# Kernel tuning notes

Measured on AMD Instinct MI355X. Metric: run time of the kernel, lower is better.

The kernel has to match this reference:

```python
import jax, jax.numpy as jnp
import numpy as np

H, N_EMB, D_EMB, D_UP = 1024, 8192, 512, 2048
B, T, BB, M, K_LABELS = 4, 4096, 512, 4096, 64


def _rms(x, w, eps=1e-6):
    xf = x.astype(jnp.float32)
    var = jnp.mean(xf * xf, axis=-1, keepdims=True)
    return (w * (xf * jax.lax.rsqrt(var + eps))).astype(x.dtype)


def setup_inputs() -> dict:
    key = jax.random.key(0)
    ks = jax.random.split(key, 8)
    bt = B * T
    inp = jax.random.normal(ks[0], (B, T, H), jnp.float32)
    w_k = jax.random.normal(ks[1], (N_EMB, H), jnp.float32) * 0.02
    w_v = jax.random.normal(ks[2], (N_EMB, D_EMB), jnp.float32) * 0.02
    w_up = jax.random.normal(ks[3], (D_UP, D_EMB), jnp.float32) * 0.02
    w_mix = jax.random.normal(ks[4], (H, D_UP + H), jnp.float32) * 0.02
    fw = jax.random.permutation(ks[5], bt)
    bw = jnp.argsort(fw)  # inverse permutation
    seq_sort = jax.random.randint(ks[6], (bt,), 0, K_LABELS)
    keep_cols = jnp.arange(M)  # keep first M of N_EMB rows
    emb_alloc = jnp.arange(N_EMB) % K_LABELS  # every label present among kept rows
    starts = jnp.zeros((bt,), jnp.int32)
    ends = jnp.full((bt,), M, jnp.int32)
    return {
        'input': inp, 'fw': fw, 'bw': bw, 'seq_sort': seq_sort,
        'keep_cols': keep_cols, 'emb_alloc': emb_alloc,
        'starts': starts, 'ends': ends, 'bb': BB,
        'w_k_weight': w_k, 'w_v_weight': w_v, 'w_up_weight': w_up,
        'w_mix_weight': w_mix,
        'norm_in_weight': jnp.ones((H,), jnp.float32),
        'norm_out_weight': jnp.ones((D_UP,), jnp.float32),
    }


def reference(input, fw, bw, seq_sort, keep_cols, emb_alloc, starts, ends, bb,
              w_k_weight, w_v_weight, w_up_weight, w_mix_weight,
              norm_in_weight, norm_out_weight):
    b, t, h = input.shape
    A = _rms(input, norm_in_weight)                      # [b,t,h]
    Bm = w_k_weight[keep_cols]                           # [m,h]
    Cm = w_v_weight[keep_cols]                           # [m,d_emb]
    la = emb_alloc[keep_cols]                            # [m]
    A = A.reshape(-1, h)[fw].reshape(-1, bb, h)          # [nb,bb,h]
    ss = seq_sort.reshape(-1, bb)                        # [nb,bb]
    st = starts.reshape(-1, bb).min(axis=-1)             # [nb]
    en = ends.reshape(-1, bb).max(axis=-1)               # [nb]
    # ragged per-block slice B[start:end] expressed as a kv range mask,
    # combined with the equality mask seq_sort[q] == emb_alloc[kv]
    scores = jnp.einsum('nqh,kh->nqk', A, Bm)            # [nb,bb,m]
    kv = jnp.arange(Bm.shape[0])
    mask = ((ss[:, :, None] == la[None, None, :])
            & (kv[None, None, :] >= st[:, None, None])
            & (kv[None, None, :] < en[:, None, None]))
    scores = jnp.where(mask, scores, -jnp.inf)
    p = jax.nn.softmax(scores, axis=-1)
    comb = jnp.einsum('nqk,kd->nqd', p, Cm)              # [nb,bb,d_emb]
    d_emb = Cm.shape[-1]
    comb = comb.reshape(-1, d_emb)[bw].reshape(b, t, d_emb)
    up = comb @ w_up_weight.T                            # [b,t,d_up]
    cat = jnp.concatenate([_rms(up, norm_out_weight), input], axis=-1)
    return cat @ w_mix_weight.T                          # [b,t,h]
```

## Files before the change

kernel.cpp:

```cpp
#include <hip/hip_runtime.h>
#include <hip/hip_bf16.h>
#include <cstdint>
#include <cstddef>

#define Hh 1024
#define D_EMB 512
#define D_UP 2048
#define BT 16384
#define BB_ 512
#define Mm 4096
#define MmP 4160
#define NB 32
#define KL 64

typedef __attribute__((ext_vector_type(4))) float f4;
typedef __attribute__((ext_vector_type(4))) __bf16 bf4;
typedef __attribute__((ext_vector_type(8))) __bf16 bf8;
typedef __attribute__((ext_vector_type(4))) float f32x4;

__device__ __forceinline__ void gl_lds16(const void* g, void* l) {
  __builtin_amdgcn_global_load_lds((__attribute__((address_space(1))) void*)g,
                                   (__attribute__((address_space(3))) void*)l, 16, 0, 0);
}

__global__ __launch_bounds__(256) void conv_bf16_kernel(const float* __restrict__ src,
                                                        __bf16* __restrict__ dst, int n4) {
  int i = blockIdx.x * 256 + threadIdx.x;
  if (i >= n4) return;
  f4 v = ((const f4*)src)[i];
  bf4 o = {(__bf16)v[0], (__bf16)v[1], (__bf16)v[2], (__bf16)v[3]};
  ((bf4*)dst)[i] = o;
}

__global__ __launch_bounds__(256) void gather_bf16_kernel(const float* __restrict__ src,
                                                          const int* __restrict__ idx,
                                                          __bf16* __restrict__ dst, int cols4) {
  int row = blockIdx.x;
  const f4* s = (const f4*)src + (size_t)idx[row] * cols4;
  bf4* d = (bf4*)dst + (size_t)row * cols4;
  for (int i = threadIdx.x; i < cols4; i += 256) {
    f4 v = s[i];
    bf4 o = {(__bf16)v[0], (__bf16)v[1], (__bf16)v[2], (__bf16)v[3]};
    d[i] = o;
  }
}

__global__ __launch_bounds__(256) void la_kernel(const int* __restrict__ keep,
                                                 const int* __restrict__ emb,
                                                 int* __restrict__ la, int m) {
  int i = blockIdx.x * 256 + threadIdx.x;
  if (i < m) la[i] = emb[keep[i]];
}

__global__ __launch_bounds__(256) void range_kernel(const int* __restrict__ starts,
                                                    const int* __restrict__ ends,
                                                    int* __restrict__ stA, int* __restrict__ enA) {
  int n = blockIdx.x;
  int t = threadIdx.x, lane = t & 63, wv = t >> 6;
  int s1 = min(starts[n * BB_ + t], starts[n * BB_ + t + 256]);
  int e1 = max(ends[n * BB_ + t], ends[n * BB_ + t + 256]);
#pragma unroll
  for (int off = 32; off; off >>= 1) {
    s1 = min(s1, __shfl_xor(s1, off));
    e1 = max(e1, __shfl_xor(e1, off));
  }
  __shared__ int ssh[4], esh[4];
  if (lane == 0) { ssh[wv] = s1; esh[wv] = e1; }
  __syncthreads();
  if (t == 0) {
    int s = ssh[0], e = esh[0];
#pragma unroll
    for (int k = 1; k < 4; ++k) { s = min(s, ssh[k]); e = max(e, esh[k]); }
    stA[n] = s; enA[n] = e;
  }
}

__global__ __launch_bounds__(256) void hist_kernel(const int* __restrict__ la,
                                                   int* __restrict__ goff) {
  __shared__ int cnt[KL];
  int tid = threadIdx.x;
  if (tid < KL) cnt[tid] = 0;
  __syncthreads();
  for (int k = tid; k < Mm; k += 256) atomicAdd(&cnt[la[k]], 1);
  __syncthreads();
  if (tid == 0) {
    int a = 0;
    for (int s = 0; s < KL; ++s) { goff[s] = a; a += cnt[s]; }
    goff[KL] = a;
  }
}

__global__ __launch_bounds__(256) void place_kernel(const int* __restrict__ la,
                                                    const int* __restrict__ keep,
                                                    const int* __restrict__ goff,
                                                    int* __restrict__ gk,
                                                    int* __restrict__ ridx) {
  int s = blockIdx.x;
  int tid = threadIdx.x, lane = tid & 63, wv = tid >> 6;
  __shared__ int wc[4];
  __shared__ int run;
  if (tid == 0) run = goff[s];
  __syncthreads();
  for (int base = 0; base < Mm; base += 256) {
    int k = base + tid;
    bool f = (la[k] == s);
    unsigned long long msk = __ballot(f);
    int myidx = __popcll(msk & ((1ull << lane) - 1ull));
    if (lane == 0) wc[wv] = __popcll(msk);
    __syncthreads();
    int woff = 0, tot = 0;
#pragma unroll
    for (int w = 0; w < 4; ++w) {
      if (w < wv) woff += wc[w];
      tot += wc[w];
    }
    int rbase = run;
    if (f) {
      int p = rbase + woff + myidx;
      gk[p] = k;
      ridx[p] = keep[k];
    }
    __syncthreads();
    if (tid == 0) run = rbase + tot;
    __syncthreads();
  }
}

__global__ __launch_bounds__(256) void lohi_kernel(const int* __restrict__ gk,
                                                   const int* __restrict__ goff,
                                                   const int* __restrict__ stA,
                                                   const int* __restrict__ enA,
                                                   int* __restrict__ loA, int* __restrict__ hiA) {
  int i = blockIdx.x * 256 + threadIdx.x;
  if (i >= NB * KL) return;
  int n = i / KL, s = i % KL;
  int b = goff[s], e = goff[s + 1];
  int st = stA[n], en = enA[n];
  int lo = b, hi = e;
  while (lo < hi) { int mid = (lo + hi) >> 1; if (gk[mid] < st) lo = mid + 1; else hi = mid; }
  int L = lo;
  lo = b; hi = e;
  while (lo < hi) { int mid = (lo + hi) >> 1; if (gk[mid] < en) lo = mid + 1; else hi = mid; }
  loA[i] = L;
  hiA[i] = lo;
}

__global__ __launch_bounds__(256) void vt_kernel(const float* __restrict__ wv_,
                                                 const int* __restrict__ ridx,
                                                 __bf16* __restrict__ VT) {
  int pb = blockIdx.x * 64;
  int db = blockIdx.y * 64;
  __shared__ float T[64][65];
  int t = threadIdx.x;
  int dl = t & 63, g = t >> 6;
  for (int i = g * 16; i < g * 16 + 16; ++i) {
    int r = ridx[pb + i];
    T[dl][i] = wv_[(size_t)r * D_EMB + db + dl];
  }
  __syncthreads();
  int pl = t & 63;
  for (int j = g * 16; j < g * 16 + 16; ++j) {
    VT[(size_t)(db + j) * MmP + pb + pl] = (__bf16)T[j][pl];
  }
}

__global__ __launch_bounds__(256) void qsort_kernel(const int* __restrict__ seq_sort,
                                                    int* __restrict__ qidx,
                                                    int* __restrict__ qoffA,
                                                    int* __restrict__ qcntA) {
  int n = blockIdx.x, tid = threadIdx.x;
  __shared__ int cnt[KL], pos[KL], pref[KL];
  if (tid < KL) cnt[tid] = 0;
  __syncthreads();
  int s0 = seq_sort[n * BB_ + tid];
  int s1 = seq_sort[n * BB_ + tid + 256];
  atomicAdd(&cnt[s0], 1);
  atomicAdd(&cnt[s1], 1);
  __syncthreads();
  if (tid == 0) {
    int a = 0;
    for (int s = 0; s < KL; ++s) { pref[s] = a; a += cnt[s]; }
  }
  __syncthreads();
  if (tid < KL) {
    pos[tid] = pref[tid];
    qoffA[n * KL + tid] = pref[tid];
    qcntA[n * KL + tid] = cnt[tid];
  }
  __syncthreads();
  int p0 = atomicAdd(&pos[s0], 1);
  qidx[n * BB_ + p0] = n * BB_ + tid;
  int p1 = atomicAdd(&pos[s1], 1);
  qidx[n * BB_ + p1] = n * BB_ + tid + 256;
}

__global__ __launch_bounds__(256) void rms_in_kernel(const float* __restrict__ input,
                                                     const int* __restrict__ fw,
                                                     const float* __restrict__ wn,
                                                     __bf16* __restrict__ Aperm,
                                                     __bf16* __restrict__ inb) {
  int wv = threadIdx.x >> 6, lane = threadIdx.x & 63;
  int j = blockIdx.x * 4 + wv;
  {
    const f4* src = (const f4*)(input + (size_t)fw[j] * Hh);
    f4 v[4];
    float ss = 0.f;
#pragma unroll
    for (int c = 0; c < 4; ++c) {
      v[c] = src[c * 64 + lane];
      ss += v[c][0] * v[c][0] + v[c][1] * v[c][1] + v[c][2] * v[c][2] + v[c][3] * v[c][3];
    }
#pragma unroll
    for (int off = 32; off; off >>= 1) ss += __shfl_xor(ss, off);
    float sc = rsqrtf(ss * (1.f / Hh) + 1e-6f);
    const f4* w4 = (const f4*)wn;
    bf4* dst = (bf4*)(Aperm + (size_t)j * Hh);
#pragma unroll
    for (int c = 0; c < 4; ++c) {
      f4 w = w4[c * 64 + lane];
      bf4 o = {(__bf16)(v[c][0] * sc * w[0]), (__bf16)(v[c][1] * sc * w[1]),
               (__bf16)(v[c][2] * sc * w[2]), (__bf16)(v[c][3] * sc * w[3])};
      dst[c * 64 + lane] = o;
    }
  }
  {
    const f4* src = (const f4*)(input + (size_t)j * Hh);
    bf4* dst = (bf4*)(inb + (size_t)j * Hh);
#pragma unroll
    for (int c = 0; c < 4; ++c) {
      f4 t = src[c * 64 + lane];
      bf4 o = {(__bf16)t[0], (__bf16)t[1], (__bf16)t[2], (__bf16)t[3]};
      dst[c * 64 + lane] = o;
    }
  }
}

__global__ __launch_bounds__(256) void attn3_kernel(const __bf16* __restrict__ Aperm,
                                                    const __bf16* __restrict__ Ks,
                                                    const __bf16* __restrict__ VT,
                                                    const int* __restrict__ qidx,
                                                    const int* __restrict__ qoffA,
                                                    const int* __restrict__ qcntA,
                                                    const int* __restrict__ loA,
                                                    const int* __restrict__ hiA,
                                                    const int* __restrict__ fw,
                                                    __bf16* __restrict__ comb) {
  int g = blockIdx.x;
  int qcnt = qcntA[g];
  if (qcnt == 0) return;
  int n = g >> 6;
  int qbase = n * BB_ + qoffA[g];
  int lo = loA[g], hi = hiA[g];
  if (lo >= hi) return;
  int tid = threadIdx.x, lane = tid & 63, wv = tid >> 6;
  int c = lane & 15, rg = lane >> 4;
  __shared__ float Sbuf[16][66];
  __shared__ __align__(16) __bf16 Plds[16][72];
  __shared__ float scl[16], lrec[16];

  for (int qt = 0; qt < qcnt; qt += 16) {
    int ql = qt + c;
    int j = qidx[qbase + (ql < qcnt ? ql : 0)];
    const __bf16* arow = Aperm + (size_t)j * Hh + rg * 8;

    float m[4] = {-1e30f, -1e30f, -1e30f, -1e30f};
    float l[4] = {0.f, 0.f, 0.f, 0.f};
    f32x4 acc[8];
    f32x4 zero = {0.f, 0.f, 0.f, 0.f};
#pragma unroll
    for (int t8 = 0; t8 < 8; ++t8) acc[t8] = zero;

    for (int p0 = lo; p0 < hi; p0 += 64) {
      int kvcol = p0 + wv * 16 + c;
      const __bf16* brow = Ks + (size_t)kvcol * Hh + rg * 8;
      f32x4 sacc = zero;
#pragma unroll
      for (int ks = 0; ks < 32; ++ks) {
        bf8 af = *(const bf8*)(arow + ks * 32);
        bf8 bf_ = *(const bf8*)(brow + ks * 32);
        sacc = __builtin_amdgcn_mfma_f32_16x16x32_bf16(af, bf_, sacc, 0, 0, 0);
      }
      bool valid = kvcol < hi;
#pragma unroll
      for (int r = 0; r < 4; ++r) Sbuf[rg * 4 + r][wv * 16 + c] = valid ? sacc[r] : -1e30f;
      __syncthreads();

#pragma unroll
      for (int r = 0; r < 4; ++r) {
        int q = wv * 4 + r;
        float s = Sbuf[q][lane];
        float cm = s;
#pragma unroll
        for (int off = 32; off; off >>= 1) cm = fmaxf(cm, __shfl_xor(cm, off));
        float mn = fmaxf(m[r], cm);
        float sc = __expf(m[r] - mn);
        float pv = __expf(s - mn);
        float ssum = pv;
#pragma unroll
        for (int off = 32; off; off >>= 1) ssum += __shfl_xor(ssum, off);
        l[r] = l[r] * sc + ssum;
        m[r] = mn;
        Plds[q][lane] = (__bf16)pv;
        if (lane == 0) scl[q] = sc;
      }
      __syncthreads();

      float sf[4];
#pragma unroll
      for (int r = 0; r < 4; ++r) sf[r] = scl[rg * 4 + r];
#pragma unroll
      for (int t8 = 0; t8 < 8; ++t8)
#pragma unroll
        for (int r = 0; r < 4; ++r) acc[t8][r] *= sf[r];

      bf8 pa0 = *(const bf8*)(&Plds[c][rg * 8]);
      bf8 pa1 = *(const bf8*)(&Plds[c][32 + rg * 8]);
#pragma unroll
      for (int tt = 0; tt < 8; ++tt) {
        int d = wv * 128 + tt * 16 + c;
        const __bf16* vrow = VT + (size_t)d * MmP + p0 + rg * 8;
        bf8 b0 = *(const bf8*)(vrow);
        bf8 b1 = *(const bf8*)(vrow + 32);
        acc[tt] = __builtin_amdgcn_mfma_f32_16x16x32_bf16(pa0, b0, acc[tt], 0, 0, 0);
        acc[tt] = __builtin_amdgcn_mfma_f32_16x16x32_bf16(pa1, b1, acc[tt], 0, 0, 0);
      }
      __syncthreads();
    }

    if (lane == 0) {
#pragma unroll
      for (int r = 0; r < 4; ++r) lrec[wv * 4 + r] = l[r];
    }
    __syncthreads();
    float inv[4];
    size_t obase[4];
    bool oval[4];
#pragma unroll
    for (int r = 0; r < 4; ++r) {
      int qq = qt + rg * 4 + r;
      oval[r] = qq < qcnt;
      int j2 = qidx[qbase + (oval[r] ? qq : 0)];
      obase[r] = (size_t)fw[j2] * D_EMB;
      float lv = lrec[rg * 4 + r];
      inv[r] = 1.f / lv;
    }
#pragma unroll
    for (int tt = 0; tt < 8; ++tt) {
      int d = wv * 128 + tt * 16 + c;
#pragma unroll
      for (int r = 0; r < 4; ++r) {
        if (oval[r]) comb[obase[r] + d] = (__bf16)(acc[tt][r] * inv[r]);
      }
    }
    __syncthreads();
  }
}

template <bool OUT_BF16>
__global__ __launch_bounds__(256, 2) void gemm_bt(const __bf16* __restrict__ x0, int k0,
                                                  const __bf16* __restrict__ x1, int k1,
                                                  const __bf16* __restrict__ w,
                                                  void* __restrict__ outp, int M, int N) {
  __shared__ __bf16 As[128 * 64];
  __shared__ __bf16 Bs[128 * 64];
  const int tid = threadIdx.x;
  const int lane = tid & 63, wv = tid >> 6;
  const int wr = wv >> 1, wc = wv & 1;
  const int m0 = blockIdx.y * 128, n0 = blockIdx.x * 128;
  const int K = k0 + k1;

  f32x4 zero = {0.f, 0.f, 0.f, 0.f};
  f32x4 acc[4][4];
#pragma unroll
  for (int a = 0; a < 4; ++a)
#pragma unroll
    for (int b = 0; b < 4; ++b) acc[a][b] = zero;

  for (int kb = 0; kb < K; kb += 64) {
    const __bf16* xs;
    int ld, kk;
    if (kb < k0) { xs = x0; ld = k0; kk = kb; }
    else         { xs = x1; ld = k1; kk = kb - k0; }
#pragma unroll
    for (int p = 0; p < 4; ++p) {
      int e = p * 256 + tid;
      int row = e >> 3, c8 = e & 7;
      gl_lds16(xs + (size_t)(m0 + row) * ld + kk + c8 * 8, (void*)(As + e * 8));
      gl_lds16(w + (size_t)(n0 + row) * K + kb + c8 * 8, (void*)(Bs + e * 8));
    }
    __syncthreads();
#pragma unroll
    for (int ks = 0; ks < 2; ++ks) {
      bf8 afr[4], bfr[4];
#pragma unroll
      for (int i = 0; i < 4; ++i) {
        afr[i] = *(const bf8*)(As + (wr * 64 + i * 16 + (lane & 15)) * 64 + ks * 32 + (lane >> 4) * 8);
        bfr[i] = *(const bf8*)(Bs + (wc * 64 + i * 16 + (lane & 15)) * 64 + ks * 32 + (lane >> 4) * 8);
      }
#pragma unroll
      for (int mi = 0; mi < 4; ++mi)
#pragma unroll
        for (int ni = 0; ni < 4; ++ni)
          acc[mi][ni] = __builtin_amdgcn_mfma_f32_16x16x32_bf16(afr[mi], bfr[ni], acc[mi][ni], 0, 0, 0);
    }
    __syncthreads();
  }
  const int r0 = (lane >> 4) * 4, cc = lane & 15;
#pragma unroll
  for (int mi = 0; mi < 4; ++mi) {
#pragma unroll
    for (int ni = 0; ni < 4; ++ni) {
      int col = n0 + wc * 64 + ni * 16 + cc;
#pragma unroll
      for (int r = 0; r < 4; ++r) {
        int row = m0 + wr * 64 + mi * 16 + r0 + r;
        float v = acc[mi][ni][r];
        if (OUT_BF16)
          ((__bf16*)outp)[(size_t)row * N + col] = (__bf16)v;
        else
          ((float*)outp)[(size_t)row * N + col] = v;
      }
    }
  }
}

__global__ __launch_bounds__(256) void rms_up_kernel(__bf16* __restrict__ up,
                                                     const float* __restrict__ wn) {
  int wv = threadIdx.x >> 6, lane = threadIdx.x & 63;
  size_t j = (size_t)blockIdx.x * 4 + wv;
  bf8* row = (bf8*)(up + j * D_UP);
  bf8 v[4];
  float ss = 0.f;
#pragma unroll
  for (int c = 0; c < 4; ++c) {
    v[c] = row[c * 64 + lane];
#pragma unroll
    for (int i = 0; i < 8; ++i) { float f = (float)v[c][i]; ss += f * f; }
  }
#pragma unroll
  for (int off = 32; off; off >>= 1) ss += __shfl_xor(ss, off);
  float sc = rsqrtf(ss * (1.f / D_UP) + 1e-6f);
#pragma unroll
  for (int c = 0; c < 4; ++c) {
    int ebase = (c * 64 + lane) * 8;
    f4 wa = *(const f4*)(wn + ebase);
    f4 wb = *(const f4*)(wn + ebase + 4);
    bf8 o;
#pragma unroll
    for (int i = 0; i < 4; ++i) o[i] = (__bf16)((float)v[c][i] * sc * wa[i]);
#pragma unroll
    for (int i = 0; i < 4; ++i) o[4 + i] = (__bf16)((float)v[c][4 + i] * sc * wb[i]);
    row[c * 64 + lane] = o;
  }
}

extern "C" void kernel_launch(void* const* d_in, const int* in_sizes, int n_in, void* d_out,
                              int out_size, void* d_ws, size_t ws_size, hipStream_t stream) {
  const float* input = (const float*)d_in[0];
  const int* fw = (const int*)d_in[1];
  const int* seq_sort = (const int*)d_in[3];
  const int* keep_cols = (const int*)d_in[4];
  const int* emb_alloc = (const int*)d_in[5];
  const int* starts = (const int*)d_in[6];
  const int* ends = (const int*)d_in[7];
  const float* w_k = (const float*)d_in[9];
  const float* w_v = (const float*)d_in[10];
  const float* w_up = (const float*)d_in[11];
  const float* w_mix = (const float*)d_in[12];
  const float* w_nin = (const float*)d_in[13];
  const float* w_nout = (const float*)d_in[14];

  char* p = (char*)d_ws;
  auto take = [&](size_t b) {
    void* r = (void*)p;
    p += (b + 255) & ~(size_t)255;
    return r;
  };
  __bf16* Aperm = (__bf16*)take((size_t)BT * Hh * 2);
  __bf16* inb = (__bf16*)take((size_t)BT * Hh * 2);
  __bf16* comb = (__bf16*)take((size_t)BT * D_EMB * 2);
  __bf16* up = (__bf16*)take((size_t)BT * D_UP * 2);
  __bf16* Ks = (__bf16*)take((size_t)MmP * Hh * 2);
  __bf16* VT = (__bf16*)take((size_t)D_EMB * MmP * 2);
  __bf16* wupB = (__bf16*)take((size_t)D_UP * D_EMB * 2);
  __bf16* wmixB = (__bf16*)take((size_t)Hh * (D_UP + Hh) * 2);
  int* la = (int*)take(Mm * 4);
  int* stA = (int*)take(NB * 4);
  int* enA = (int*)take(NB * 4);
  int* goff = (int*)take((KL + 1) * 4);
  int* gk = (int*)take(Mm * 4);
  int* ridx = (int*)take(Mm * 4);
  int* loA = (int*)take(NB * KL * 4);
  int* hiA = (int*)take(NB * KL * 4);
  int* qidx = (int*)take(BT * 4);
  int* qoffA = (int*)take(NB * KL * 4);
  int* qcntA = (int*)take(NB * KL * 4);

  conv_bf16_kernel<<<(D_UP * D_EMB / 4 + 255) / 256, 256, 0, stream>>>(w_up, wupB, D_UP * D_EMB / 4);
  conv_bf16_kernel<<<(Hh * (D_UP + Hh) / 4 + 255) / 256, 256, 0, stream>>>(w_mix, wmixB,
                                                                           Hh * (D_UP + Hh) / 4);
  la_kernel<<<Mm / 256, 256, 0, stream>>>(keep_cols, emb_alloc, la, Mm);
  range_kernel<<<NB, 256, 0, stream>>>(starts, ends, stA, enA);
  hist_kernel<<<1, 256, 0, stream>>>(la, goff);
  place_kernel<<<KL, 256, 0, stream>>>(la, keep_cols, goff, gk, ridx);
  lohi_kernel<<<(NB * KL + 255) / 256, 256, 0, stream>>>(gk, goff, stA, enA, loA, hiA);
  gather_bf16_kernel<<<Mm, 256, 0, stream>>>(w_k, ridx, Ks, Hh / 4);
  vt_kernel<<<dim3(Mm / 64, D_EMB / 64), 256, 0, stream>>>(w_v, ridx, VT);
  qsort_kernel<<<NB, 256, 0, stream>>>(seq_sort, qidx, qoffA, qcntA);

  rms_in_kernel<<<BT / 4, 256, 0, stream>>>(input, fw, w_nin, Aperm, inb);
  attn3_kernel<<<NB * KL, 256, 0, stream>>>(Aperm, Ks, VT, qidx, qoffA, qcntA, loA, hiA, fw, comb);
  gemm_bt<true><<<dim3(D_UP / 128, BT / 128), 256, 0, stream>>>(comb, D_EMB, (const __bf16*)nullptr,
                                                                0, wupB, (void*)up, BT, D_UP);
  rms_up_kernel<<<BT / 4, 256, 0, stream>>>(up, w_nout);
  gemm_bt<false><<<dim3(Hh / 128, BT / 128), 256, 0, stream>>>(up, D_UP, inb, Hh, wmixB, d_out, BT,
                                                               Hh);
}
```

Before: 364.8 us.

## Rewrite GEMM with 256x256 tiles, 4-stage LDS pipeline, swizzle and XCD mapping

Replaces the 128x128 single-buffered GEMM with a 512-thread kernel that computes 256x256 tiles. It uses a 4-deep ring of K=32 LDS stages filled by global_load_lds, an XOR-swizzled LDS layout to avoid bank conflicts, s_setprio around the MFMA bursts, and block-index remapping across the 8 XCDs for L2 locality. The goal is to overlap global loads with MFMA work and raise data reuse per tile. In exchange it uses more registers and LDS per block, and the grid is smaller (64x4 blocks for the second GEMM), which may leave CUs idle.

```diff
diff --git a/kernel.cpp b/kernel.cpp
--- a/kernel.cpp
+++ b/kernel.cpp
@@ -12,6 +12,7 @@
 #define MmP 4160
 #define NB 32
 #define KL 64
+#define NXCD 8
 
 typedef __attribute__((ext_vector_type(4))) float f4;
 typedef __attribute__((ext_vector_type(4))) __bf16 bf4;
@@ -357,68 +358,101 @@
 }
 
 template <bool OUT_BF16>
-__global__ __launch_bounds__(256, 2) void gemm_bt(const __bf16* __restrict__ x0, int k0,
-                                                  const __bf16* __restrict__ x1, int k1,
-                                                  const __bf16* __restrict__ w,
-                                                  void* __restrict__ outp, int M, int N) {
-  __shared__ __bf16 As[128 * 64];
-  __shared__ __bf16 Bs[128 * 64];
-  const int tid = threadIdx.x;
-  const int lane = tid & 63, wv = tid >> 6;
-  const int wr = wv >> 1, wc = wv & 1;
-  const int m0 = blockIdx.y * 128, n0 = blockIdx.x * 128;
+__global__ __launch_bounds__(512, 2) void gemm8p(const __bf16* __restrict__ x0, int k0,
+                                                 const __bf16* __restrict__ x1, int k1,
+                                                 const __bf16* __restrict__ w,
+                                                 void* __restrict__ outp, int Mt, int Nt) {
+  __shared__ __align__(16) __bf16 lds[4][2][256 * 32];
+  const int nwg = Mt * Nt;
+  const int bid = blockIdx.x;
+  const int swz = (bid % NXCD) * (nwg / NXCD) + bid / NXCD;
+  const int m0 = (swz / Nt) * 256, n0 = (swz % Nt) * 256;
   const int K = k0 + k1;
-
-  f32x4 zero = {0.f, 0.f, 0.f, 0.f};
-  f32x4 acc[4][4];
-#pragma unroll
-  for (int a = 0; a < 4; ++a)
-#pragma unroll
-    for (int b = 0; b < 4; ++b) acc[a][b] = zero;
-
-  for (int kb = 0; kb < K; kb += 64) {
+  const int NT = K >> 5;
+  const int N = Nt * 256;
+  const int tid = threadIdx.x, lane = tid & 63, wvi = tid >> 6;
+  const int wr = wvi >> 2, wc = wvi & 3;
+
+  const int srow = tid >> 2;
+  const int spb = (tid & 3) * 16;
+
+  const int c = lane & 15, rg = lane >> 4;
+  const int fa_off = c * 64 + ((rg ^ ((c >> 1) & 3)) << 4);
+
+  auto stage_half = [&](int t, int j) {
+    int kg = t * 32;
     const __bf16* xs;
     int ld, kk;
-    if (kb < k0) { xs = x0; ld = k0; kk = kb; }
-    else         { xs = x1; ld = k1; kk = kb - k0; }
-#pragma unroll
-    for (int p = 0; p < 4; ++p) {
-      int e = p * 256 + tid;
-      int row = e >> 3, c8 = e & 7;
-      gl_lds16(xs + (size_t)(m0 + row) * ld + kk + c8 * 8, (void*)(As + e * 8));
-      gl_lds16(w + (size_t)(n0 + row) * K + kb + c8 * 8, (void*)(Bs + e * 8));
-    }
-    __syncthreads();
-#pragma unroll
-    for (int ks = 0; ks < 2; ++ks) {
-      bf8 afr[4], bfr[4];
-#pragma unroll
-      for (int i = 0; i < 4; ++i) {
-        afr[i] = *(const bf8*)(As + (wr * 64 + i * 16 + (lane & 15)) * 64 + ks * 32 + (lane >> 4) * 8);
-        bfr[i] = *(const bf8*)(Bs + (wc * 64 + i * 16 + (lane & 15)) * 64 + ks * 32 + (lane >> 4) * 8);
+    if (kg < k0) { xs = x0; ld = k0; kk = kg; }
+    else         { xs = x1; ld = k1; kk = kg - k0; }
+    int b = t & 3;
+    int r = j * 128 + srow;
+    int lcol = (spb ^ (((r >> 1) & 3) << 4)) >> 1;
+    gl_lds16(xs + (size_t)(m0 + r) * ld + kk + lcol,
+             (void*)((char*)&lds[b][0][0] + r * 64 + spb));
+    gl_lds16(w + (size_t)(n0 + r) * K + kg + lcol,
+             (void*)((char*)&lds[b][1][0] + r * 64 + spb));
+  };
+
+  f32x4 acc[8][4];
+  f32x4 zero = {0.f, 0.f, 0.f, 0.f};
+#pragma unroll
+  for (int a = 0; a < 8; ++a)
+#pragma unroll
+    for (int bnx = 0; bnx < 4; ++bnx) acc[a][bnx] = zero;
+
+#pragma unroll
+  for (int t = 0; t < 3; ++t) {
+    stage_half(t, 0);
+    stage_half(t, 1);
+  }
+  asm volatile("s_waitcnt vmcnt(8)" ::: "memory");
+  __builtin_amdgcn_s_barrier();
+
+  for (int t = 0; t < NT; ++t) {
+    const char* Abase = (const char*)&lds[t & 3][0][0];
+    const char* Bbase = (const char*)&lds[t & 3][1][0];
+    bf8 bfr[4];
+#pragma unroll
+    for (int ri = 0; ri < 2; ++ri) {
+      if (t + 3 < NT) stage_half(t + 3, ri);
+      bf8 afr[4];
+#pragma unroll
+      for (int fi = 0; fi < 4; ++fi)
+        afr[fi] = *(const bf8*)(Abase + (wr * 128 + ri * 64 + fi * 16) * 64 + fa_off);
+      if (ri == 0) {
+#pragma unroll
+        for (int fi = 0; fi < 4; ++fi)
+          bfr[fi] = *(const bf8*)(Bbase + (wc * 64 + fi * 16) * 64 + fa_off);
       }
-#pragma unroll
-      for (int mi = 0; mi < 4; ++mi)
+      __builtin_amdgcn_s_barrier();
+      __builtin_amdgcn_s_setprio(1);
+#pragma unroll
+      for (int fi = 0; fi < 4; ++fi)
 #pragma unroll
         for (int ni = 0; ni < 4; ++ni)
-          acc[mi][ni] = __builtin_amdgcn_mfma_f32_16x16x32_bf16(afr[mi], bfr[ni], acc[mi][ni], 0, 0, 0);
-    }
-    __syncthreads();
-  }
+          acc[ri * 4 + fi][ni] =
+              __builtin_amdgcn_mfma_f32_16x16x32_bf16(afr[fi], bfr[ni], acc[ri * 4 + fi][ni], 0, 0, 0);
+      __builtin_amdgcn_s_setprio(0);
+      if (ri == 1) asm volatile("s_waitcnt vmcnt(8)" ::: "memory");
+      __builtin_amdgcn_s_barrier();
+    }
+  }
+
   const int r0 = (lane >> 4) * 4, cc = lane & 15;
 #pragma unroll
-  for (int mi = 0; mi < 4; ++mi) {
+  for (int mi = 0; mi < 8; ++mi) {
+    int rowb = m0 + wr * 128 + (mi >> 2) * 64 + (mi & 3) * 16 + r0;
 #pragma unroll
     for (int ni = 0; ni < 4; ++ni) {
       int col = n0 + wc * 64 + ni * 16 + cc;
 #pragma unroll
       for (int r = 0; r < 4; ++r) {
-        int row = m0 + wr * 64 + mi * 16 + r0 + r;
         float v = acc[mi][ni][r];
         if (OUT_BF16)
-          ((__bf16*)outp)[(size_t)row * N + col] = (__bf16)v;
+          ((__bf16*)outp)[(size_t)(rowb + r) * N + col] = (__bf16)v;
         else
-          ((float*)outp)[(size_t)row * N + col] = v;
+          ((float*)outp)[(size_t)(rowb + r) * N + col] = v;
       }
     }
   }
@@ -510,9 +544,9 @@
 
   rms_in_kernel<<<BT / 4, 256, 0, stream>>>(input, fw, w_nin, Aperm, inb);
   attn3_kernel<<<NB * KL, 256, 0, stream>>>(Aperm, Ks, VT, qidx, qoffA, qcntA, loA, hiA, fw, comb);
-  gemm_bt<true><<<dim3(D_UP / 128, BT / 128), 256, 0, stream>>>(comb, D_EMB, (const __bf16*)nullptr,
-                                                                0, wupB, (void*)up, BT, D_UP);
+  gemm8p<true><<<BT / 256 * (D_UP / 256), 512, 0, stream>>>(comb, D_EMB, (const __bf16*)nullptr, 0,
+                                                            wupB, (void*)up, BT / 256, D_UP / 256);
   rms_up_kernel<<<BT / 4, 256, 0, stream>>>(up, w_nout);
-  gemm_bt<false><<<dim3(Hh / 128, BT / 128), 256, 0, stream>>>(up, D_UP, inb, Hh, wmixB, d_out, BT,
-                                                               Hh);
-}
+  gemm8p<false><<<BT / 256 * (Hh / 256), 512, 0, stream>>>(up, D_UP, inb, Hh, wmixB, d_out,
+                                                           BT / 256, Hh / 256);
+}
```

After: 332.9 us. 1.1x faster.
